# Performance work log

Measured on AMD Instinct MI355X. Metric: run time of the kernel, lower is better.

## Reference

```python
import jax, jax.numpy as jnp
import numpy as np
import math

C = 256
NUM_CLASSES = 80
NUM_CONVS = 4
GROUPS = 32
LEVEL_SHAPES = [(100, 152), (50, 76), (25, 38), (13, 19), (7, 10)]
BATCH = 2


def conv2d(x, w, b):
    # x: [N,C,H,W], w: [O,I,3,3] -> SAME padding, stride 1
    y = jax.lax.conv_general_dilated(x, w, window_strides=(1, 1), padding='SAME',
                                     dimension_numbers=('NCHW', 'OIHW', 'NCHW'))
    return y + b[None, :, None, None]


def group_norm(x, w, b, groups=GROUPS, eps=1e-5):
    N, Ch, H, W = x.shape
    xg = x.reshape(N, groups, Ch // groups, H, W)
    mu = jnp.mean(xg, axis=(2, 3, 4), keepdims=True)
    var = jnp.var(xg, axis=(2, 3, 4), keepdims=True)
    xg = (xg - mu) * jax.lax.rsqrt(var + eps)
    x = xg.reshape(N, Ch, H, W)
    return x * w[None, :, None, None] + b[None, :, None, None]


def tower(x, cw, cb, gw, gb):
    for i in range(NUM_CONVS):
        x = jax.nn.relu(group_norm(conv2d(x, cw[i], cb[i]), gw[i], gb[i]))
    return x


def flatten_head(y, c):
    # [N, A*c, H, W] -> [N, H*W*A, c]  (matches view/permute/reshape in torch)
    N, AC, H, W = y.shape
    A = AC // c
    return y.reshape(N, A, c, H, W).transpose(0, 3, 4, 1, 2).reshape(N, H * W * A, c)


def setup_inputs() -> dict:
    key = jax.random.key(0)
    ks = iter(jax.random.split(key, 64))
    inp = {}
    for i, (h, w) in enumerate(LEVEL_SHAPES):
        inp[f"feat{i}"] = jax.random.normal(next(ks), (BATCH, C, h, w), jnp.float32)
    def cw(shape):  # conv weights init std=0.01 as in torch module
        return jax.random.normal(next(ks), shape, jnp.float32) * 0.01
    inp["cls_conv_w"] = cw((NUM_CONVS, C, C, 3, 3))
    inp["cls_conv_b"] = jnp.zeros((NUM_CONVS, C), jnp.float32)
    inp["cls_gn_w"] = jnp.ones((NUM_CONVS, C), jnp.float32)
    inp["cls_gn_b"] = jnp.zeros((NUM_CONVS, C), jnp.float32)
    inp["cls_out_w"] = cw((NUM_CLASSES, C, 3, 3))
    inp["cls_out_b"] = jnp.full((NUM_CLASSES,), -math.log(99.0), jnp.float32)  # prior prob 0.01
    inp["reg_conv_w"] = cw((NUM_CONVS, C, C, 3, 3))
    inp["reg_conv_b"] = jnp.zeros((NUM_CONVS, C), jnp.float32)
    inp["reg_gn_w"] = jnp.ones((NUM_CONVS, C), jnp.float32)
    inp["reg_gn_b"] = jnp.zeros((NUM_CONVS, C), jnp.float32)
    for name, oc in [("bbox", 4), ("ctr", 1), ("dim", 3), ("ori", 1), ("kp", 16), ("depth", 1)]:
        inp[f"{name}_w"] = cw((oc, C, 3, 3))
        inp[f"{name}_b"] = jnp.zeros((oc,), jnp.float32)
    return inp


def reference(feat0, feat1, feat2, feat3, feat4,
              cls_conv_w, cls_conv_b, cls_gn_w, cls_gn_b, cls_out_w, cls_out_b,
              reg_conv_w, reg_conv_b, reg_gn_w, reg_gn_b,
              bbox_w, bbox_b, ctr_w, ctr_b, dim_w, dim_b,
              ori_w, ori_b, kp_w, kp_b, depth_w, depth_b):
    feats = [feat0, feat1, feat2, feat3, feat4]
    cls_all, bbox_all, ctr_all, dim_all, ori_all, kp_all, depth_all = ([] for _ in range(7))
    for f in feats:
        cf = tower(f, cls_conv_w, cls_conv_b, cls_gn_w, cls_gn_b)
        cls_all.append(flatten_head(conv2d(cf, cls_out_w, cls_out_b), NUM_CLASSES))
        rf = tower(f, reg_conv_w, reg_conv_b, reg_gn_w, reg_gn_b)
        bbox_all.append(flatten_head(jax.nn.relu(conv2d(rf, bbox_w, bbox_b)), 4))
        ctr_all.append(flatten_head(conv2d(rf, ctr_w, ctr_b), 1))
        dim_all.append(flatten_head(conv2d(rf, dim_w, dim_b), 3))
        ori_all.append(flatten_head(conv2d(rf, ori_w, ori_b), 1))
        kp_all.append(flatten_head(conv2d(rf, kp_w, kp_b), 16))
        depth_all.append(flatten_head(conv2d(rf, depth_w, depth_b), 1))
    cat = lambda xs: jnp.concatenate(xs, axis=1)
    return (cat(cls_all), cat(bbox_all), cat(ctr_all), cat(dim_all),
            cat(ori_all), cat(kp_all), cat(depth_all))
```

## Files before the change

kernel.cpp:

```cpp
#include <hip/hip_runtime.h>
#include <stdint.h>

typedef unsigned short ushort_t;
typedef __bf16 bf16x8 __attribute__((ext_vector_type(8)));
typedef float f32x4 __attribute__((ext_vector_type(4)));

#define TOTAL_HW 20267
#define PTOT 21267

__constant__ int d_RB[26] = {3242720,3242720,3242720,3242720, 3404856, 3445390,3445390,3445390,
                             3566992, 3607526,3607526,3607526,3607526,3607526,3607526,3607526,3607526,
                             3607526,3607526,3607526,3607526,3607526,3607526,3607526,3607526, 4256070};
__constant__ int d_RM[26] = {4,4,4,4, 1, 3,3,3, 1, 16,16,16,16,16,16,16,16,16,16,16,16,16,16,16,16, 1};
__constant__ int d_RC[26] = {0,1,2,3, 0, 0,1,2, 0, 0,1,2,3,4,5,6,7,8,9,10,11,12,13,14,15, 0};

__constant__ int F_TC[6]   = {0,238,298,314,318,320};
__constant__ int F_TL[5]   = {119,30,8,2,1};
__constant__ int F_W[5]    = {152,76,38,19,10};
__constant__ int F_HW[5]   = {15200,3800,950,247,70};
__constant__ int F_PB[5]   = {0,15708,19764,20844,21159};
__constant__ int F_LOFF[5] = {0,15200,19000,19950,20197};
__constant__ int F_PC[6]   = {0,508,764,894,962,1000};
__constant__ int F_H[5]    = {100,50,25,13,7};

__device__ __forceinline__ ushort_t f2bf(float f) {
    union { float f; uint32_t i; } x; x.f = f;
    uint32_t r = x.i + 0x7fffu + ((x.i >> 16) & 1u);
    return (ushort_t)(r >> 16);
}
__device__ __forceinline__ float bf2f(ushort_t u) {
    union { uint32_t i; float f; } x; x.i = ((uint32_t)u) << 16; return x.f;
}
__device__ __forceinline__ void gld16(const ushort_t* g, ushort_t* lds) {
    __builtin_amdgcn_global_load_lds((const __attribute__((address_space(1))) void*)g,
                                     (__attribute__((address_space(3))) void*)lds, 16, 0, 0);
}

__global__ __launch_bounds__(256) void wtrans_tower_k(const float* __restrict__ src,
                                                      ushort_t* __restrict__ dst)
{
    int id = blockIdx.x * 256 + threadIdx.x;
    int oc = id >> 8, ic = id & 255;
    const float* s = src + (size_t)(oc * 256 + ic) * 9;
    ushort_t* d = dst + oc * 256 + ic;
    #pragma unroll
    for (int t = 0; t < 9; t++) d[t * 65536] = f2bf(s[t]);
}
__global__ __launch_bounds__(256) void wtrans_cls_k(const float* __restrict__ src,
                                                    ushort_t* __restrict__ dst)
{
    int id = blockIdx.x * 256 + threadIdx.x;
    int oc = id >> 8, ic = id & 255;
    ushort_t* d = dst + oc * 256 + ic;
    if (oc < 80) {
        const float* s = src + (size_t)(oc * 256 + ic) * 9;
        #pragma unroll
        for (int t = 0; t < 9; t++) d[t * 32768] = f2bf(s[t]);
    } else {
        #pragma unroll
        for (int t = 0; t < 9; t++) d[t * 32768] = 0;
    }
}
__global__ __launch_bounds__(256) void wtrans_reg_k(
    const float* bbox_w, const float* ctr_w, const float* dim_w,
    const float* ori_w,  const float* kp_w,  const float* depth_w,
    const float* bbox_b, const float* ctr_b, const float* dim_b,
    const float* ori_b,  const float* kp_b,  const float* depth_b,
    ushort_t* __restrict__ dst, float* __restrict__ RegBias)
{
    int id = blockIdx.x * 256 + threadIdx.x;
    int oc = id >> 8, ic = id & 255;
    ushort_t* d = dst + oc * 256 + ic;
    if (oc < 26) {
        const float* s; int c;
        if (oc < 4)       { s = bbox_w;  c = oc; }
        else if (oc < 5)  { s = ctr_w;   c = 0; }
        else if (oc < 8)  { s = dim_w;   c = oc - 5; }
        else if (oc < 9)  { s = ori_w;   c = 0; }
        else if (oc < 25) { s = kp_w;    c = oc - 9; }
        else              { s = depth_w; c = 0; }
        const float* sp = s + (size_t)(c * 256 + ic) * 9;
        #pragma unroll
        for (int t = 0; t < 9; t++) d[t * 32768] = f2bf(sp[t]);
    } else {
        #pragma unroll
        for (int t = 0; t < 9; t++) d[t * 32768] = 0;
    }
    if (id < 26) {
        const float* b; int c;
        if (id < 4)       { b = bbox_b;  c = id; }
        else if (id < 5)  { b = ctr_b;   c = 0; }
        else if (id < 8)  { b = dim_b;   c = id - 5; }
        else if (id < 9)  { b = ori_b;   c = 0; }
        else if (id < 25) { b = kp_b;    c = id - 9; }
        else              { b = depth_b; c = 0; }
        RegBias[id] = b[c];
    }
}

__global__ __launch_bounds__(256) void pad_k(ushort_t* b0, ushort_t* b1, ushort_t* b2, ushort_t* b3)
{
    int u = blockIdx.x * 256 + threadIdx.x;
    if (u >= 256000) return;
    int chunk = u & 31; u >>= 5;
    int buf = u & 3; u >>= 2;
    int n = (u >= 1000) ? 1 : 0; int pidx = u - n * 1000;
    int l = 0;
    #pragma unroll
    for (int i = 1; i < 5; i++) if (pidx >= F_PC[i]) l = i;
    int q = pidx - F_PC[l];
    int W = F_W[l], H = F_H[l], Wp = W + 2;
    int py, px;
    if (q < Wp) { py = 0; px = q; }
    else if (q < 2 * Wp) { py = H + 1; px = q - Wp; }
    else { int q2 = q - 2 * Wp; py = 1 + (q2 >> 1); px = (q2 & 1) ? (Wp - 1) : 0; }
    ushort_t* base = b0;
    if (buf == 1) base = b1; else if (buf == 2) base = b2; else if (buf == 3) base = b3;
    *(uint4*)(base + ((size_t)n * PTOT + F_PB[l] + py * Wp + px) * 256 + chunk * 8) = uint4{0u,0u,0u,0u};
}

__global__ __launch_bounds__(256) void packF_k(
    const float* f0, const float* f1, const float* f2,
    const float* f3, const float* f4, ushort_t* __restrict__ S)
{
    __shared__ ushort_t tile[64][65];
    const int PCUM[6] = {0, 1904, 2384, 2504, 2536, 2552};
    const int PT[5]   = {238, 60, 15, 4, 2};
    int bid = blockIdx.x;
    int l = 0;
    #pragma unroll
    for (int i = 1; i < 5; i++) if (bid >= PCUM[i]) l = i;
    int r = bid - PCUM[l];
    int per_n = PT[l] * 4;
    int n = (r >= per_n) ? 1 : 0; r -= n * per_n;
    int pb = r >> 2, cb = r & 3;
    const float* fs = f0;
    if (l == 1) fs = f1; else if (l == 2) fs = f2; else if (l == 3) fs = f3; else if (l == 4) fs = f4;
    int HW = F_HW[l], W = F_W[l], Wp = W + 2;
    int p0 = pb * 64, c0 = cb * 64;
    int t = threadIdx.x;
    #pragma unroll
    for (int i = 0; i < 16; i++) {
        int idx = i * 256 + t; int cl = idx >> 6, pl = idx & 63;
        int p = p0 + pl; ushort_t v = 0;
        if (p < HW) v = f2bf(fs[(size_t)(n * 256 + c0 + cl) * HW + p]);
        tile[cl][pl] = v;
    }
    __syncthreads();
    ushort_t* ob = S + ((size_t)n * PTOT + F_PB[l]) * 256;
    #pragma unroll
    for (int i = 0; i < 16; i++) {
        int idx = i * 256 + t; int pl = idx >> 6, cl = idx & 63;
        int p = p0 + pl;
        if (p < HW) {
            int y = p / W, x = p - y * W;
            ob[((y + 1) * Wp + (x + 1)) * 256 + c0 + cl] = tile[cl][pl];
        }
    }
}

__global__ __launch_bounds__(256) void convT_k(
    const ushort_t* __restrict__ srcC, const ushort_t* __restrict__ srcR,
    ushort_t* __restrict__ dstC, ushort_t* __restrict__ dstR,
    const ushort_t* __restrict__ wtAll,
    const float* __restrict__ biasC, const float* __restrict__ biasR,
    float* __restrict__ stats, int L)
{
    __shared__ __align__(16) ushort_t As[3][4096];
    __shared__ __align__(16) ushort_t Bs[3][4096];

    int gid = blockIdx.x;
    int xcd = gid & 7, idx = gid >> 3;
    int bid = xcd * 40 + (idx >> 2);
    int oc0 = (idx & 1) * 128;
    int tw = (idx >> 1) & 1;

    const ushort_t* src = tw ? srcR : srcC;
    ushort_t* dst = tw ? dstR : dstC;
    const ushort_t* wt = wtAll + (size_t)(tw * 4 + L) * 589824;
    const float* bias = (tw ? biasR : biasC) + L * 256;

    int l = 0;
    #pragma unroll
    for (int i = 1; i < 5; i++) if (bid >= F_TC[i]) l = i;
    int r = bid - F_TC[l];
    int tl = F_TL[l];
    int n = (r >= tl) ? 1 : 0; int tile = r - n * tl;
    int W = F_W[l], HW = F_HW[l], Wp = W + 2;
    int px0 = tile * 128;
    const ushort_t* sbase = src + ((size_t)n * PTOT + F_PB[l]) * 256;
    ushort_t* obase = dst + ((size_t)n * PTOT + F_PB[l]) * 256;

    int tid = threadIdx.x, wv = tid >> 6, ln = tid & 63;
    int wr = wv >> 1, wc = wv & 1;

    int aoff[2], boff[2];
    #pragma unroll
    for (int j = 0; j < 2; j++) {
        int rloc = (wv * 2 + j) * 16 + (ln >> 2);
        int p = px0 + rloc; if (p > HW - 1) p = HW - 1;
        int y = p / W, x = p - y * W;
        int c = ((ln & 3) - (rloc >> 1)) & 3;
        aoff[j] = ((y + 1) * Wp + (x + 1)) * 256 + c * 8;
        boff[j] = (oc0 + rloc) * 256 + c * 8;
    }

    f32x4 acc[4][4];
    #pragma unroll
    for (int mi = 0; mi < 4; mi++)
        #pragma unroll
        for (int ni = 0; ni < 4; ni++) acc[mi][ni] = f32x4{0.f, 0.f, 0.f, 0.f};

    {
        int tapo = (-Wp - 1) * 256;
        #pragma unroll
        for (int j = 0; j < 2; j++) gld16(sbase + aoff[j] + tapo, &As[0][(wv * 2 + j) * 512]);
        #pragma unroll
        for (int j = 0; j < 2; j++) gld16(wt + boff[j], &Bs[0][(wv * 2 + j) * 512]);
        asm volatile("" ::: "memory");
        #pragma unroll
        for (int j = 0; j < 2; j++) gld16(sbase + aoff[j] + tapo + 32, &As[1][(wv * 2 + j) * 512]);
        #pragma unroll
        for (int j = 0; j < 2; j++) gld16(wt + 32 + boff[j], &Bs[1][(wv * 2 + j) * 512]);
    }

    #pragma unroll 3
    for (int it = 0; it < 72; ++it) {
        if (it < 71) {
            asm volatile("s_waitcnt vmcnt(4) lgkmcnt(0)\n\ts_barrier" ::: "memory");
        } else {
            asm volatile("s_waitcnt vmcnt(0) lgkmcnt(0)\n\ts_barrier" ::: "memory");
        }
        int nx = it + 2;
        if (nx < 72) {
            int tp = nx >> 3, kc = (nx & 7) << 5;
            int ky = tp / 3, kx = tp - ky * 3;
            int tapo = ((ky - 1) * Wp + (kx - 1)) * 256 + kc;
            const ushort_t* wtap = wt + tp * 65536 + kc;
            int bs = nx % 3;
            #pragma unroll
            for (int j = 0; j < 2; j++) gld16(sbase + aoff[j] + tapo, &As[bs][(wv * 2 + j) * 512]);
            #pragma unroll
            for (int j = 0; j < 2; j++) gld16(wtap + boff[j], &Bs[bs][(wv * 2 + j) * 512]);
        }
        int b = it % 3;
        bf16x8 af[4], bg[4];
        #pragma unroll
        for (int mi = 0; mi < 4; mi++) {
            int rA = wr * 64 + mi * 16 + (ln & 15);
            int ch = ((ln >> 4) + (rA >> 1)) & 3;
            af[mi] = *(const bf16x8*)&As[b][rA * 32 + ch * 8];
        }
        #pragma unroll
        for (int ni = 0; ni < 4; ni++) {
            int rB = wc * 64 + ni * 16 + (ln & 15);
            int ch = ((ln >> 4) + (rB >> 1)) & 3;
            bg[ni] = *(const bf16x8*)&Bs[b][rB * 32 + ch * 8];
        }
        __builtin_amdgcn_s_setprio(1);
        #pragma unroll
        for (int mi = 0; mi < 4; mi++)
            #pragma unroll
            for (int ni = 0; ni < 4; ni++)
                acc[mi][ni] = __builtin_amdgcn_mfma_f32_16x16x32_bf16(af[mi], bg[ni], acc[mi][ni], 0, 0, 0);
        __builtin_amdgcn_s_setprio(0);
    }

    #pragma unroll
    for (int ni = 0; ni < 4; ni++) {
        int oc = oc0 + wc * 64 + ni * 16 + (ln & 15);
        float bv = bias[oc];
        float s = 0.f, q = 0.f;
        #pragma unroll
        for (int mi = 0; mi < 4; mi++) {
            int pb = px0 + wr * 64 + mi * 16 + ((ln >> 4) << 2);
            if (pb < HW) {
                int y = pb / W, x = pb - y * W;
                #pragma unroll
                for (int rr2 = 0; rr2 < 4; rr2++) {
                    int p = pb + rr2;
                    if (p < HW) {
                        float v = acc[mi][ni][rr2] + bv;
                        obase[((y + 1) * Wp + (x + 1)) * 256 + oc] = f2bf(v);
                        s += v; q += v * v;
                    }
                    x++; if (x == W) { x = 0; y++; }
                }
            }
        }
        s += __shfl_xor(s, 16, 64); q += __shfl_xor(q, 16, 64);
        s += __shfl_xor(s, 32, 64); q += __shfl_xor(q, 32, 64);
        s += __shfl_xor(s, 1, 64);  q += __shfl_xor(q, 1, 64);
        s += __shfl_xor(s, 2, 64);  q += __shfl_xor(q, 2, 64);
        s += __shfl_xor(s, 4, 64);  q += __shfl_xor(q, 4, 64);
        if (ln == 0 || ln == 8) {
            int g = (oc0 + wc * 64 + ni * 16 + (ln & 8)) >> 3;
            float* st = stats + (size_t)((tw * 4 + L) * 5 + l) * 128 + (n * 32 + g) * 2;
            atomicAdd(st, s); atomicAdd(st + 1, q);
        }
    }
}

__global__ __launch_bounds__(256) void convH_k(
    const ushort_t* __restrict__ srcC, const ushort_t* __restrict__ srcR,
    const ushort_t* __restrict__ wtC, const ushort_t* __restrict__ wtR,
    const float* __restrict__ biasC, const float* __restrict__ biasR,
    float* __restrict__ outF)
{
    __shared__ __align__(16) ushort_t As[3][4096];
    __shared__ __align__(16) ushort_t Bs[3][4096];

    int gid = blockIdx.x;
    int xcd = gid & 7, idx = gid >> 3;
    int bid = xcd * 40 + (idx >> 1);
    int mode = idx & 1;

    const ushort_t* src = mode ? srcR : srcC;
    const ushort_t* wt  = mode ? wtR  : wtC;
    const float* bias   = mode ? biasR : biasC;

    int l = 0;
    #pragma unroll
    for (int i = 1; i < 5; i++) if (bid >= F_TC[i]) l = i;
    int r = bid - F_TC[l];
    int tl = F_TL[l];
    int n = (r >= tl) ? 1 : 0; int tile = r - n * tl;
    int W = F_W[l], HW = F_HW[l], Wp = W + 2;
    int px0 = tile * 128;
    const ushort_t* sbase = src + ((size_t)n * PTOT + F_PB[l]) * 256;

    int tid = threadIdx.x, wv = tid >> 6, ln = tid & 63;
    int wr = wv >> 1, wc = wv & 1;

    int aoff[2], boff[2];
    #pragma unroll
    for (int j = 0; j < 2; j++) {
        int rloc = (wv * 2 + j) * 16 + (ln >> 2);
        int p = px0 + rloc; if (p > HW - 1) p = HW - 1;
        int y = p / W, x = p - y * W;
        int c = ((ln & 3) - (rloc >> 1)) & 3;
        aoff[j] = ((y + 1) * Wp + (x + 1)) * 256 + c * 8;
        boff[j] = rloc * 256 + c * 8;
    }

    f32x4 acc[4][4];
    #pragma unroll
    for (int mi = 0; mi < 4; mi++)
        #pragma unroll
        for (int ni = 0; ni < 4; ni++) acc[mi][ni] = f32x4{0.f, 0.f, 0.f, 0.f};

    {
        int tapo = (-Wp - 1) * 256;
        #pragma unroll
        for (int j = 0; j < 2; j++) gld16(sbase + aoff[j] + tapo, &As[0][(wv * 2 + j) * 512]);
        #pragma unroll
        for (int j = 0; j < 2; j++) gld16(wt + boff[j], &Bs[0][(wv * 2 + j) * 512]);
        asm volatile("" ::: "memory");
        #pragma unroll
        for (int j = 0; j < 2; j++) gld16(sbase + aoff[j] + tapo + 32, &As[1][(wv * 2 + j) * 512]);
        #pragma unroll
        for (int j = 0; j < 2; j++) gld16(wt + 32 + boff[j], &Bs[1][(wv * 2 + j) * 512]);
    }

    #pragma unroll 3
    for (int it = 0; it < 72; ++it) {
        if (it < 71) {
            asm volatile("s_waitcnt vmcnt(4) lgkmcnt(0)\n\ts_barrier" ::: "memory");
        } else {
            asm volatile("s_waitcnt vmcnt(0) lgkmcnt(0)\n\ts_barrier" ::: "memory");
        }
        int nx = it + 2;
        if (nx < 72) {
            int tp = nx >> 3, kc = (nx & 7) << 5;
            int ky = tp / 3, kx = tp - ky * 3;
            int tapo = ((ky - 1) * Wp + (kx - 1)) * 256 + kc;
            const ushort_t* wtap = wt + tp * 32768 + kc;
            int bs = nx % 3;
            #pragma unroll
            for (int j = 0; j < 2; j++) gld16(sbase + aoff[j] + tapo, &As[bs][(wv * 2 + j) * 512]);
            #pragma unroll
            for (int j = 0; j < 2; j++) gld16(wtap + boff[j], &Bs[bs][(wv * 2 + j) * 512]);
        }
        int b = it % 3;
        bf16x8 af[4], bg[4];
        #pragma unroll
        for (int mi = 0; mi < 4; mi++) {
            int rA = wr * 64 + mi * 16 + (ln & 15);
            int ch = ((ln >> 4) + (rA >> 1)) & 3;
            af[mi] = *(const bf16x8*)&As[b][rA * 32 + ch * 8];
        }
        #pragma unroll
        for (int ni = 0; ni < 4; ni++) {
            int rB = wc * 64 + ni * 16 + (ln & 15);
            int ch = ((ln >> 4) + (rB >> 1)) & 3;
            bg[ni] = *(const bf16x8*)&Bs[b][rB * 32 + ch * 8];
        }
        __builtin_amdgcn_s_setprio(1);
        #pragma unroll
        for (int mi = 0; mi < 4; mi++)
            #pragma unroll
            for (int ni = 0; ni < 4; ni++)
                acc[mi][ni] = __builtin_amdgcn_mfma_f32_16x16x32_bf16(af[mi], bg[ni], acc[mi][ni], 0, 0, 0);
        __builtin_amdgcn_s_setprio(0);
    }

    #pragma unroll
    for (int ni = 0; ni < 4; ni++) {
        int oc = wc * 64 + ni * 16 + (ln & 15);
        bool valid = mode ? (oc < 26) : (oc < 80);
        if (valid) {
            float bv = bias[oc];
            int rb = 0, rm = 80, rc = oc; bool rl = false;
            if (mode) { rb = d_RB[oc]; rm = d_RM[oc]; rc = d_RC[oc]; rl = (oc < 4); }
            #pragma unroll
            for (int mi = 0; mi < 4; mi++) {
                int pb = px0 + wr * 64 + mi * 16 + ((ln >> 4) << 2);
                #pragma unroll
                for (int rr2 = 0; rr2 < 4; rr2++) {
                    int p = pb + rr2;
                    if (p < HW) {
                        float v = acc[mi][ni][rr2] + bv;
                        if (rl) v = fmaxf(v, 0.f);
                        int pg = n * TOTAL_HW + F_LOFF[l] + p;
                        outF[rb + (size_t)pg * rm + rc] = v;
                    }
                }
            }
        }
    }
}

__global__ __launch_bounds__(256) void normF_k(
    ushort_t* __restrict__ bufC, ushort_t* __restrict__ bufR,
    const float* __restrict__ stats,
    const float* __restrict__ gwC, const float* __restrict__ gwR,
    const float* __restrict__ gbC, const float* __restrict__ gbR, int L)
{
    int u = blockIdx.x * 256 + threadIdx.x;
    if (u >= 2594176) return;
    int tw = (u >= 1297088) ? 1 : 0; u -= tw * 1297088;
    int n = (u >= 648544) ? 1 : 0; u -= n * 648544;
    int cp = u >> 5, g = u & 31;
    int l = 0;
    #pragma unroll
    for (int i = 1; i < 5; i++) if (cp >= F_LOFF[i]) l = i;
    int p = cp - F_LOFF[l];
    int W = F_W[l], HW = F_HW[l];
    int y = p / W, x = p - y * W;
    const float* st = stats + (size_t)((tw * 4 + L) * 5 + l) * 128 + (n * 32 + g) * 2;
    float cnt = 8.0f * (float)HW;
    float mean = st[0] / cnt;
    float var = st[1] / cnt - mean * mean;
    float inv = rsqrtf(fmaxf(var, 0.f) + 1e-5f);
    const float* gw = (tw ? gwR : gwC) + L * 256 + g * 8;
    const float* gb = (tw ? gbR : gbC) + L * 256 + g * 8;
    ushort_t* buf = tw ? bufR : bufC;
    ushort_t* ptr = buf + (((size_t)n * PTOT + F_PB[l]) + (y + 1) * (W + 2) + (x + 1)) * 256 + g * 8;
    uint4 din = *(const uint4*)ptr;
    uint4 dout;
    const ushort_t* xi = (const ushort_t*)&din;
    ushort_t* oi = (ushort_t*)&dout;
    #pragma unroll
    for (int i = 0; i < 8; i++) {
        float v = (bf2f(xi[i]) - mean) * inv * gw[i] + gb[i];
        oi[i] = f2bf(fmaxf(v, 0.f));
    }
    *(uint4*)ptr = dout;
}


extern "C" void kernel_launch(void* const* d_in, const int* in_sizes, int n_in,
                              void* d_out, int out_size, void* d_ws, size_t ws_size,
                              hipStream_t stream) {
    const float* feats[5] = {(const float*)d_in[0], (const float*)d_in[1],
                             (const float*)d_in[2], (const float*)d_in[3],
                             (const float*)d_in[4]};
    const float* cls_conv_w = (const float*)d_in[5];
    const float* cls_conv_b = (const float*)d_in[6];
    const float* cls_gn_w   = (const float*)d_in[7];
    const float* cls_gn_b   = (const float*)d_in[8];
    const float* cls_out_w  = (const float*)d_in[9];
    const float* cls_out_b  = (const float*)d_in[10];
    const float* reg_conv_w = (const float*)d_in[11];
    const float* reg_conv_b = (const float*)d_in[12];
    const float* reg_gn_w   = (const float*)d_in[13];
    const float* reg_gn_b   = (const float*)d_in[14];

    char* wsb = (char*)d_ws;
    float* Stats     = (float*)wsb;
    float* RegBias   = (float*)(wsb + 20480);
    ushort_t* TowerWtAll = (ushort_t*)(wsb + 20608);
    ushort_t* WtCls  = (ushort_t*)(wsb + 9457792);
    ushort_t* WtReg  = (ushort_t*)(wsb + 10047616);
    ushort_t* S  = (ushort_t*)(wsb + 10637440);
    ushort_t* Ac = (ushort_t*)(wsb + 32414848);
    ushort_t* Ar = (ushort_t*)(wsb + 54192256);
    ushort_t* Br = (ushort_t*)(wsb + 75969664);
    float* outf  = (float*)d_out;

    hipMemsetAsync(d_ws, 0, 20608, stream);
    pad_k<<<1000, 256, 0, stream>>>(S, Ac, Ar, Br);

    for (int tw = 0; tw < 2; tw++) {
        const float* conv_w = tw ? reg_conv_w : cls_conv_w;
        for (int L = 0; L < 4; L++)
            wtrans_tower_k<<<256, 256, 0, stream>>>(conv_w + (size_t)L * 589824,
                                                    TowerWtAll + (size_t)(tw * 4 + L) * 589824);
    }
    wtrans_cls_k<<<128, 256, 0, stream>>>(cls_out_w, WtCls);
    wtrans_reg_k<<<128, 256, 0, stream>>>(
        (const float*)d_in[15], (const float*)d_in[17], (const float*)d_in[19],
        (const float*)d_in[21], (const float*)d_in[23], (const float*)d_in[25],
        (const float*)d_in[16], (const float*)d_in[18], (const float*)d_in[20],
        (const float*)d_in[22], (const float*)d_in[24], (const float*)d_in[26],
        WtReg, RegBias);

    packF_k<<<2552, 256, 0, stream>>>(feats[0], feats[1], feats[2], feats[3], feats[4], S);

    ushort_t* sc[4] = {S,  Ac, S,  Ac};
    ushort_t* dc[4] = {Ac, S,  Ac, S };
    ushort_t* sr[4] = {S,  Ar, Br, Ar};
    ushort_t* dr[4] = {Ar, Br, Ar, Br};
    for (int L = 0; L < 4; L++) {
        convT_k<<<1280, 256, 0, stream>>>(
            sc[L], sr[L], dc[L], dr[L], TowerWtAll, cls_conv_b, reg_conv_b, Stats, L);
        normF_k<<<10134, 256, 0, stream>>>(
            dc[L], dr[L], Stats, cls_gn_w, reg_gn_w, cls_gn_b, reg_gn_b, L);
    }
    convH_k<<<640, 256, 0, stream>>>(S, Br, WtCls, WtReg, cls_out_b, RegBias, outf);
}
```

Measured before the change: 911.0 us.

## Use 8 waves per block in conv GEMMs and merge tower weight transposes

The tower and head conv kernels go from 4 to 8 waves per block. Each wave now computes a 64x32 tile instead of 64x64 and issues one A and one B LDS load per stage instead of two. This halves the accumulator registers per wave and doubles the waves available to hide MFMA and load latency. Eight tower weight-transpose launches are also merged into one grid. The cost is more barrier participants and less MFMA reuse of each A fragment per LDS read.

```diff
diff --git a/kernel.cpp b/kernel.cpp
--- a/kernel.cpp
+++ b/kernel.cpp
@@ -36,13 +36,17 @@
                                      (__attribute__((address_space(3))) void*)lds, 16, 0, 0);
 }
 
-__global__ __launch_bounds__(256) void wtrans_tower_k(const float* __restrict__ src,
-                                                      ushort_t* __restrict__ dst)
+__global__ __launch_bounds__(256) void wtrans_towerall_k(const float* __restrict__ cw,
+                                                         const float* __restrict__ rw,
+                                                         ushort_t* __restrict__ dst)
 {
     int id = blockIdx.x * 256 + threadIdx.x;
-    int oc = id >> 8, ic = id & 255;
-    const float* s = src + (size_t)(oc * 256 + ic) * 9;
-    ushort_t* d = dst + oc * 256 + ic;
+    int g = id >> 16;
+    int oc = (id >> 8) & 255, ic = id & 255;
+    const float* base = (g >= 4) ? rw : cw;
+    int L = g & 3;
+    const float* s = base + (size_t)L * 589824 + (size_t)(oc * 256 + ic) * 9;
+    ushort_t* d = dst + (size_t)g * 589824 + oc * 256 + ic;
     #pragma unroll
     for (int t = 0; t < 9; t++) d[t * 65536] = f2bf(s[t]);
 }
@@ -159,7 +163,7 @@
     }
 }
 
-__global__ __launch_bounds__(256) void convT_k(
+__global__ __launch_bounds__(512, 4) void convT_k(
     const ushort_t* __restrict__ srcC, const ushort_t* __restrict__ srcR,
     ushort_t* __restrict__ dstC, ushort_t* __restrict__ dstR,
     const ushort_t* __restrict__ wtAll,
@@ -192,42 +196,37 @@
     ushort_t* obase = dst + ((size_t)n * PTOT + F_PB[l]) * 256;
 
     int tid = threadIdx.x, wv = tid >> 6, ln = tid & 63;
-    int wr = wv >> 1, wc = wv & 1;
-
-    int aoff[2], boff[2];
-    #pragma unroll
-    for (int j = 0; j < 2; j++) {
-        int rloc = (wv * 2 + j) * 16 + (ln >> 2);
+    int wr = wv >> 2, wc = wv & 3;
+
+    int aoff, boff;
+    {
+        int rloc = wv * 16 + (ln >> 2);
         int p = px0 + rloc; if (p > HW - 1) p = HW - 1;
         int y = p / W, x = p - y * W;
         int c = ((ln & 3) - (rloc >> 1)) & 3;
-        aoff[j] = ((y + 1) * Wp + (x + 1)) * 256 + c * 8;
-        boff[j] = (oc0 + rloc) * 256 + c * 8;
-    }
-
-    f32x4 acc[4][4];
+        aoff = ((y + 1) * Wp + (x + 1)) * 256 + c * 8;
+        boff = (oc0 + rloc) * 256 + c * 8;
+    }
+
+    f32x4 acc[4][2];
     #pragma unroll
     for (int mi = 0; mi < 4; mi++)
         #pragma unroll
-        for (int ni = 0; ni < 4; ni++) acc[mi][ni] = f32x4{0.f, 0.f, 0.f, 0.f};
+        for (int ni = 0; ni < 2; ni++) acc[mi][ni] = f32x4{0.f, 0.f, 0.f, 0.f};
 
     {
         int tapo = (-Wp - 1) * 256;
-        #pragma unroll
-        for (int j = 0; j < 2; j++) gld16(sbase + aoff[j] + tapo, &As[0][(wv * 2 + j) * 512]);
-        #pragma unroll
-        for (int j = 0; j < 2; j++) gld16(wt + boff[j], &Bs[0][(wv * 2 + j) * 512]);
+        gld16(sbase + aoff + tapo, &As[0][wv * 512]);
+        gld16(wt + boff, &Bs[0][wv * 512]);
         asm volatile("" ::: "memory");
-        #pragma unroll
-        for (int j = 0; j < 2; j++) gld16(sbase + aoff[j] + tapo + 32, &As[1][(wv * 2 + j) * 512]);
-        #pragma unroll
-        for (int j = 0; j < 2; j++) gld16(wt + 32 + boff[j], &Bs[1][(wv * 2 + j) * 512]);
+        gld16(sbase + aoff + tapo + 32, &As[1][wv * 512]);
+        gld16(wt + 32 + boff, &Bs[1][wv * 512]);
     }
 
     #pragma unroll 3
     for (int it = 0; it < 72; ++it) {
         if (it < 71) {
-            asm volatile("s_waitcnt vmcnt(4) lgkmcnt(0)\n\ts_barrier" ::: "memory");
+            asm volatile("s_waitcnt vmcnt(2) lgkmcnt(0)\n\ts_barrier" ::: "memory");
         } else {
             asm volatile("s_waitcnt vmcnt(0) lgkmcnt(0)\n\ts_barrier" ::: "memory");
         }
@@ -238,13 +237,11 @@
             int tapo = ((ky - 1) * Wp + (kx - 1)) * 256 + kc;
             const ushort_t* wtap = wt + tp * 65536 + kc;
             int bs = nx % 3;
-            #pragma unroll
-            for (int j = 0; j < 2; j++) gld16(sbase + aoff[j] + tapo, &As[bs][(wv * 2 + j) * 512]);
-            #pragma unroll
-            for (int j = 0; j < 2; j++) gld16(wtap + boff[j], &Bs[bs][(wv * 2 + j) * 512]);
+            gld16(sbase + aoff + tapo, &As[bs][wv * 512]);
+            gld16(wtap + boff, &Bs[bs][wv * 512]);
         }
         int b = it % 3;
-        bf16x8 af[4], bg[4];
+        bf16x8 af[4], bg[2];
         #pragma unroll
         for (int mi = 0; mi < 4; mi++) {
             int rA = wr * 64 + mi * 16 + (ln & 15);
@@ -252,8 +249,8 @@
             af[mi] = *(const bf16x8*)&As[b][rA * 32 + ch * 8];
         }
         #pragma unroll
-        for (int ni = 0; ni < 4; ni++) {
-            int rB = wc * 64 + ni * 16 + (ln & 15);
+        for (int ni = 0; ni < 2; ni++) {
+            int rB = wc * 32 + ni * 16 + (ln & 15);
             int ch = ((ln >> 4) + (rB >> 1)) & 3;
             bg[ni] = *(const bf16x8*)&Bs[b][rB * 32 + ch * 8];
         }
@@ -261,14 +258,14 @@
         #pragma unroll
         for (int mi = 0; mi < 4; mi++)
             #pragma unroll
-            for (int ni = 0; ni < 4; ni++)
+            for (int ni = 0; ni < 2; ni++)
                 acc[mi][ni] = __builtin_amdgcn_mfma_f32_16x16x32_bf16(af[mi], bg[ni], acc[mi][ni], 0, 0, 0);
         __builtin_amdgcn_s_setprio(0);
     }
 
     #pragma unroll
-    for (int ni = 0; ni < 4; ni++) {
-        int oc = oc0 + wc * 64 + ni * 16 + (ln & 15);
+    for (int ni = 0; ni < 2; ni++) {
+        int oc = oc0 + wc * 32 + ni * 16 + (ln & 15);
         float bv = bias[oc];
         float s = 0.f, q = 0.f;
         #pragma unroll
@@ -294,14 +291,14 @@
         s += __shfl_xor(s, 2, 64);  q += __shfl_xor(q, 2, 64);
         s += __shfl_xor(s, 4, 64);  q += __shfl_xor(q, 4, 64);
         if (ln == 0 || ln == 8) {
-            int g = (oc0 + wc * 64 + ni * 16 + (ln & 8)) >> 3;
+            int g = (oc0 + wc * 32 + ni * 16 + (ln & 8)) >> 3;
             float* st = stats + (size_t)((tw * 4 + L) * 5 + l) * 128 + (n * 32 + g) * 2;
             atomicAdd(st, s); atomicAdd(st + 1, q);
         }
     }
 }
 
-__global__ __launch_bounds__(256) void convH_k(
+__global__ __launch_bounds__(512, 4) void convH_k(
     const ushort_t* __restrict__ srcC, const ushort_t* __restrict__ srcR,
     const ushort_t* __restrict__ wtC, const ushort_t* __restrict__ wtR,
     const float* __restrict__ biasC, const float* __restrict__ biasR,
@@ -330,42 +327,37 @@
     const ushort_t* sbase = src + ((size_t)n * PTOT + F_PB[l]) * 256;
 
     int tid = threadIdx.x, wv = tid >> 6, ln = tid & 63;
-    int wr = wv >> 1, wc = wv & 1;
-
-    int aoff[2], boff[2];
-    #pragma unroll
-    for (int j = 0; j < 2; j++) {
-        int rloc = (wv * 2 + j) * 16 + (ln >> 2);
+    int wr = wv >> 2, wc = wv & 3;
+
+    int aoff, boff;
+    {
+        int rloc = wv * 16 + (ln >> 2);
         int p = px0 + rloc; if (p > HW - 1) p = HW - 1;
         int y = p / W, x = p - y * W;
         int c = ((ln & 3) - (rloc >> 1)) & 3;
-        aoff[j] = ((y + 1) * Wp + (x + 1)) * 256 + c * 8;
-        boff[j] = rloc * 256 + c * 8;
-    }
-
-    f32x4 acc[4][4];
+        aoff = ((y + 1) * Wp + (x + 1)) * 256 + c * 8;
+        boff = rloc * 256 + c * 8;
+    }
+
+    f32x4 acc[4][2];
     #pragma unroll
     for (int mi = 0; mi < 4; mi++)
         #pragma unroll
-        for (int ni = 0; ni < 4; ni++) acc[mi][ni] = f32x4{0.f, 0.f, 0.f, 0.f};
+        for (int ni = 0; ni < 2; ni++) acc[mi][ni] = f32x4{0.f, 0.f, 0.f, 0.f};
 
     {
         int tapo = (-Wp - 1) * 256;
-        #pragma unroll
-        for (int j = 0; j < 2; j++) gld16(sbase + aoff[j] + tapo, &As[0][(wv * 2 + j) * 512]);
-        #pragma unroll
-        for (int j = 0; j < 2; j++) gld16(wt + boff[j], &Bs[0][(wv * 2 + j) * 512]);
+        gld16(sbase + aoff + tapo, &As[0][wv * 512]);
+        gld16(wt + boff, &Bs[0][wv * 512]);
         asm volatile("" ::: "memory");
-        #pragma unroll
-        for (int j = 0; j < 2; j++) gld16(sbase + aoff[j] + tapo + 32, &As[1][(wv * 2 + j) * 512]);
-        #pragma unroll
-        for (int j = 0; j < 2; j++) gld16(wt + 32 + boff[j], &Bs[1][(wv * 2 + j) * 512]);
+        gld16(sbase + aoff + tapo + 32, &As[1][wv * 512]);
+        gld16(wt + 32 + boff, &Bs[1][wv * 512]);
     }
 
     #pragma unroll 3
     for (int it = 0; it < 72; ++it) {
         if (it < 71) {
-            asm volatile("s_waitcnt vmcnt(4) lgkmcnt(0)\n\ts_barrier" ::: "memory");
+            asm volatile("s_waitcnt vmcnt(2) lgkmcnt(0)\n\ts_barrier" ::: "memory");
         } else {
             asm volatile("s_waitcnt vmcnt(0) lgkmcnt(0)\n\ts_barrier" ::: "memory");
         }
@@ -376,13 +368,11 @@
             int tapo = ((ky - 1) * Wp + (kx - 1)) * 256 + kc;
             const ushort_t* wtap = wt + tp * 32768 + kc;
             int bs = nx % 3;
-            #pragma unroll
-            for (int j = 0; j < 2; j++) gld16(sbase + aoff[j] + tapo, &As[bs][(wv * 2 + j) * 512]);
-            #pragma unroll
-            for (int j = 0; j < 2; j++) gld16(wtap + boff[j], &Bs[bs][(wv * 2 + j) * 512]);
+            gld16(sbase + aoff + tapo, &As[bs][wv * 512]);
+            gld16(wtap + boff, &Bs[bs][wv * 512]);
         }
         int b = it % 3;
-        bf16x8 af[4], bg[4];
+        bf16x8 af[4], bg[2];
         #pragma unroll
         for (int mi = 0; mi < 4; mi++) {
             int rA = wr * 64 + mi * 16 + (ln & 15);
@@ -390,8 +380,8 @@
             af[mi] = *(const bf16x8*)&As[b][rA * 32 + ch * 8];
         }
         #pragma unroll
-        for (int ni = 0; ni < 4; ni++) {
-            int rB = wc * 64 + ni * 16 + (ln & 15);
+        for (int ni = 0; ni < 2; ni++) {
+            int rB = wc * 32 + ni * 16 + (ln & 15);
             int ch = ((ln >> 4) + (rB >> 1)) & 3;
             bg[ni] = *(const bf16x8*)&Bs[b][rB * 32 + ch * 8];
         }
@@ -399,14 +389,14 @@
         #pragma unroll
         for (int mi = 0; mi < 4; mi++)
             #pragma unroll
-            for (int ni = 0; ni < 4; ni++)
+            for (int ni = 0; ni < 2; ni++)
                 acc[mi][ni] = __builtin_amdgcn_mfma_f32_16x16x32_bf16(af[mi], bg[ni], acc[mi][ni], 0, 0, 0);
         __builtin_amdgcn_s_setprio(0);
     }
 
     #pragma unroll
-    for (int ni = 0; ni < 4; ni++) {
-        int oc = wc * 64 + ni * 16 + (ln & 15);
+    for (int ni = 0; ni < 2; ni++) {
+        int oc = wc * 32 + ni * 16 + (ln & 15);
         bool valid = mode ? (oc < 26) : (oc < 80);
         if (valid) {
             float bv = bias[oc];
@@ -501,12 +491,7 @@
     hipMemsetAsync(d_ws, 0, 20608, stream);
     pad_k<<<1000, 256, 0, stream>>>(S, Ac, Ar, Br);
 
-    for (int tw = 0; tw < 2; tw++) {
-        const float* conv_w = tw ? reg_conv_w : cls_conv_w;
-        for (int L = 0; L < 4; L++)
-            wtrans_tower_k<<<256, 256, 0, stream>>>(conv_w + (size_t)L * 589824,
-                                                    TowerWtAll + (size_t)(tw * 4 + L) * 589824);
-    }
+    wtrans_towerall_k<<<2048, 256, 0, stream>>>(cls_conv_w, reg_conv_w, TowerWtAll);
     wtrans_cls_k<<<128, 256, 0, stream>>>(cls_out_w, WtCls);
     wtrans_reg_k<<<128, 256, 0, stream>>>(
         (const float*)d_in[15], (const float*)d_in[17], (const float*)d_in[19],
@@ -522,10 +507,10 @@
     ushort_t* sr[4] = {S,  Ar, Br, Ar};
     ushort_t* dr[4] = {Ar, Br, Ar, Br};
     for (int L = 0; L < 4; L++) {
-        convT_k<<<1280, 256, 0, stream>>>(
+        convT_k<<<1280, 512, 0, stream>>>(
             sc[L], sr[L], dc[L], dr[L], TowerWtAll, cls_conv_b, reg_conv_b, Stats, L);
         normF_k<<<10134, 256, 0, stream>>>(
             dc[L], dr[L], Stats, cls_gn_w, reg_gn_w, cls_gn_b, reg_gn_b, L);
     }
-    convH_k<<<640, 256, 0, stream>>>(S, Br, WtCls, WtReg, cls_out_b, RegBias, outf);
-}
+    convH_k<<<640, 512, 0, stream>>>(S, Br, WtCls, WtReg, cls_out_b, RegBias, outf);
+}
```

Result: faster. 890.3 us (-2.3%).
